# Optimization experiments

Measured on AMD Instinct MI355X. Metric: run time of the kernel, lower is better.

The kernel has to match this reference:

```python
import jax, jax.numpy as jnp
import numpy as np

N_NODES = 50000
N_EDGES = 800000
IN_FEATS = 128
OUT_FEATS = 64


def setup_inputs() -> dict:
    key = jax.random.key(0)
    k1, k2, k3, k4, k5, k6 = jax.random.split(key, 6)
    feat = jax.random.normal(k1, (N_NODES, IN_FEATS), dtype=jnp.float32)
    edge_src = jax.random.randint(k2, (N_EDGES,), 0, N_NODES, dtype=jnp.int64)
    edge_dst = jax.random.randint(k3, (N_EDGES,), 0, N_NODES, dtype=jnp.int64)
    eweight = jax.random.uniform(k4, (N_EDGES,), dtype=jnp.float32)
    W = jax.random.normal(k5, (OUT_FEATS, IN_FEATS), dtype=jnp.float32) * (1.0 / np.sqrt(IN_FEATS))
    b = jax.random.normal(k6, (OUT_FEATS,), dtype=jnp.float32) * 0.01
    return {"feat": feat, "edge_src": edge_src, "edge_dst": edge_dst,
            "eweight": eweight, "W": W, "b": b}


def reference(feat, edge_src, edge_dst, eweight, W, b):
    # Linear: [N, in] @ [in, out] + [out]
    h = jnp.einsum('ni,oi->no', feat, W) + b
    # u_mul_e: gather src features, scale by per-edge weight -> [E, out]
    m = h[edge_src] * eweight[:, None]
    # sum reduce over dst -> [N, out]
    out = jax.ops.segment_sum(m, edge_dst, num_segments=N_NODES)
    return out
```

## Files before the change

kernel.cpp:

```cpp
#include <hip/hip_runtime.h>

#define IN_FEATS 128
#define OUT_FEATS 64
#define TM 64
#define ALD 136
#define BW_LOG 6
#define BWIDTH 64
#define MAX_NB 1024
#define SE_PER_BLK 2048
#define CAP 2048
#define MAXR 4

typedef short bf16x8 __attribute__((ext_vector_type(8)));
typedef float f32x4 __attribute__((ext_vector_type(4)));

__device__ inline unsigned short f2bf(float f) {
    unsigned u = __float_as_uint(f);
    u += 0x7FFFu + ((u >> 16) & 1u);
    return (unsigned short)(u >> 16);
}
__device__ inline float bf2f_lo(unsigned v) { return __uint_as_float(v << 16); }
__device__ inline float bf2f_hi(unsigned v) { return __uint_as_float(v & 0xFFFF0000u); }
__device__ inline ushort4 cvt4(float4 t) {
    ushort4 s; s.x = f2bf(t.x); s.y = f2bf(t.y); s.z = f2bf(t.z); s.w = f2bf(t.w);
    return s;
}

__global__ __launch_bounds__(256) void stage_linear(
    const float* __restrict__ feat, const float* __restrict__ W,
    const float* __restrict__ b, unsigned short* __restrict__ h,
    const int* __restrict__ esrc, const int* __restrict__ edst,
    const float* __restrict__ ew, int* __restrict__ gcur,
    int2* __restrict__ gstage, int n_nodes, int n_edges, int nb, int nstage)
{
    __shared__ union {
        struct { unsigned short As[TM * ALD]; unsigned short Ws[OUT_FEATS * ALD]; } lin;
        struct { int cnt[MAX_NB]; int base[MAX_NB]; } st;
    } sm;
    const int tid = threadIdx.x;

    if ((int)blockIdx.x < nstage) {
        int* cnt  = sm.st.cnt;
        int* base = sm.st.base;
        for (int i = tid; i < nb; i += 256) cnt[i] = 0;
        __syncthreads();

        const int e0 = blockIdx.x * SE_PER_BLK + tid * 8;
        int dk[8]; int sk[8]; float wk[8]; int bk[8]; int rk[8];
        if (e0 + 7 < n_edges) {
            *((int4*)&dk[0]) = *((const int4*)&edst[e0]);
            *((int4*)&dk[4]) = *((const int4*)&edst[e0 + 4]);
            *((int4*)&sk[0]) = *((const int4*)&esrc[e0]);
            *((int4*)&sk[4]) = *((const int4*)&esrc[e0 + 4]);
            *((float4*)&wk[0]) = *((const float4*)&ew[e0]);
            *((float4*)&wk[4]) = *((const float4*)&ew[e0 + 4]);
#pragma unroll
            for (int i = 0; i < 8; ++i) {
                bk[i] = dk[i] >> BW_LOG;
                rk[i] = atomicAdd(&cnt[bk[i]], 1);
            }
        } else {
#pragma unroll
            for (int i = 0; i < 8; ++i) {
                int e = e0 + i;
                if (e < n_edges) {
                    dk[i] = edst[e]; sk[i] = esrc[e]; wk[i] = ew[e];
                    bk[i] = dk[i] >> BW_LOG;
                    rk[i] = atomicAdd(&cnt[bk[i]], 1);
                } else bk[i] = -1;
            }
        }
        __syncthreads();
        for (int i = tid; i < nb; i += 256) {
            int c = cnt[i];
            base[i] = c ? atomicAdd(&gcur[i], c) : 0;
        }
        __syncthreads();
#pragma unroll
        for (int i = 0; i < 8; ++i) {
            if (bk[i] >= 0) {
                int off = base[bk[i]] + rk[i];
                if (off < CAP)
                    gstage[bk[i] * CAP + off] =
                        make_int2(((dk[i] & (BWIDTH - 1)) << 16) | sk[i],
                                  __float_as_int(wk[i]));
            }
        }
    } else {
        unsigned short* As = sm.lin.As;
        unsigned short* Ws = sm.lin.Ws;
        const int row0 = ((int)blockIdx.x - nstage) * TM;

        {
            const int c  = tid & 63;
            const int kb = (tid >> 6) * 32;
            const float4* wrow = (const float4*)(W + (size_t)c * IN_FEATS + kb);
#pragma unroll
            for (int i = 0; i < 8; ++i)
                *((ushort4*)&Ws[c * ALD + kb + i * 4]) = cvt4(wrow[i]);
        }
        {
#pragma unroll
            for (int i = 0; i < 8; ++i) {
                int flat = i * 256 + tid;
                int r  = flat >> 5;
                int kc = flat & 31;
                int gr = row0 + r;
                float4 t = (gr < n_nodes)
                    ? ((const float4*)(feat + (size_t)gr * IN_FEATS))[kc]
                    : make_float4(0.f, 0.f, 0.f, 0.f);
                *((ushort4*)&As[r * ALD + kc * 4]) = cvt4(t);
            }
        }
        __syncthreads();

        const int w    = tid >> 6;
        const int lane = tid & 63;
        const int m    = lane & 15;
        const int quad = lane >> 4;
        const int koff = quad * 8;

        f32x4 acc[4];
#pragma unroll
        for (int t = 0; t < 4; ++t) acc[t] = (f32x4){0.f, 0.f, 0.f, 0.f};

#pragma unroll
        for (int chunk = 0; chunk < 4; ++chunk) {
            const int kc = chunk * 32 + koff;
            bf16x8 a = *((const bf16x8*)&As[(w * 16 + m) * ALD + kc]);
#pragma unroll
            for (int t = 0; t < 4; ++t) {
                bf16x8 bfr = *((const bf16x8*)&Ws[(t * 16 + m) * ALD + kc]);
                acc[t] = __builtin_amdgcn_mfma_f32_16x16x32_bf16(a, bfr, acc[t], 0, 0, 0);
            }
        }

#pragma unroll
        for (int t = 0; t < 4; ++t) {
            const int col = t * 16 + m;
            const float bias = b[col];
#pragma unroll
            for (int i = 0; i < 4; ++i) {
                int r = row0 + w * 16 + quad * 4 + i;
                if (r < n_nodes)
                    h[(size_t)r * OUT_FEATS + col] = f2bf(acc[t][i] + bias);
            }
        }
    }
}

__global__ __launch_bounds__(512) void sort_gather(
    const unsigned short* __restrict__ h, const int* __restrict__ gcnt,
    const int2* __restrict__ gstage, float* __restrict__ out, int n_nodes)
{
    __shared__ int2 srec[CAP];
    __shared__ int cnt[BWIDTH];
    __shared__ int cur0[BWIDTH];
    __shared__ int cur[BWIDTH];
    const int tid = threadIdx.x;
    const int b   = blockIdx.x;
    const int s0  = b * CAP;
    const int m   = min(gcnt[b], CAP);

    if (tid < BWIDTH) cnt[tid] = 0;
    __syncthreads();

    int2 rl[MAXR];
#pragma unroll
    for (int k = 0; k < MAXR; ++k) {
        int i = tid + k * 512;
        if (i < m) {
            rl[k] = gstage[s0 + i];
            atomicAdd(&cnt[(rl[k].x >> 16) & 63], 1);
        }
    }
    __syncthreads();

    if (tid < 64) {
        int v = cnt[tid];
        int inc = v;
        for (int o = 1; o < 64; o <<= 1) {
            int t = __shfl_up(inc, o, 64);
            if (tid >= o) inc += t;
        }
        int excl = inc - v;
        cur0[tid] = excl;
        cur[tid]  = excl;
    }
    __syncthreads();

#pragma unroll
    for (int k = 0; k < MAXR; ++k) {
        int i = tid + k * 512;
        if (i < m) {
            int pos = atomicAdd(&cur[(rl[k].x >> 16) & 63], 1);
            srec[pos] = rl[k];
        }
    }
    __syncthreads();

    const int lane = tid & 63;
    const int wv   = tid >> 6;
    const int g    = lane >> 4;
    const int f4   = lane & 15;
    const uint2* h64 = (const uint2*)h;

#pragma unroll
    for (int it = 0; it < 2; ++it) {
        const int nl   = wv * 8 + it * 4 + g;
        const int node = b * BWIDTH + nl;
        const int st   = cur0[nl];
        const int len  = cnt[nl];
        int omax = len;
        omax = max(omax, __shfl_xor(omax, 16, 64));
        omax = max(omax, __shfl_xor(omax, 32, 64));

        float a0 = 0.f, a1 = 0.f, a2 = 0.f, a3 = 0.f;
        for (int u = 0; u < omax; u += 8) {
            int2 r[8]; uint2 hv[8];
#pragma unroll
            for (int k = 0; k < 8; ++k) {
                int uk = u + k;
                r[k] = srec[(uk < len) ? (st + uk) : 0];
            }
#pragma unroll
            for (int k = 0; k < 8; ++k)
                hv[k] = h64[(size_t)(r[k].x & 0xFFFF) * 16 + f4];
#pragma unroll
            for (int k = 0; k < 8; ++k) {
                float w = (u + k < len) ? __int_as_float(r[k].y) : 0.f;
                a0 += w * bf2f_lo(hv[k].x);
                a1 += w * bf2f_hi(hv[k].x);
                a2 += w * bf2f_lo(hv[k].y);
                a3 += w * bf2f_hi(hv[k].y);
            }
        }
        if (node < n_nodes) {
            float4 o; o.x = a0; o.y = a1; o.z = a2; o.w = a3;
            *((float4*)&out[(size_t)node * OUT_FEATS + f4 * 4]) = o;
        }
    }
}

__global__ __launch_bounds__(256) void scatter_kernel(
    const unsigned short* __restrict__ h, const int* __restrict__ esrc,
    const int* __restrict__ edst, const float* __restrict__ ew,
    float* __restrict__ out, int n_edges)
{
    const int lane = threadIdx.x & 63;
    const int wave = threadIdx.x >> 6;
    const int stride = gridDim.x * 4;
    for (int e = blockIdx.x * 4 + wave; e < n_edges; e += stride) {
        const int s = esrc[e];
        const int d = edst[e];
        const float w = ew[e];
        atomicAdd(out + (size_t)d * OUT_FEATS + lane,
                  bf2f_lo((unsigned)h[(size_t)s * OUT_FEATS + lane]) * w);
    }
}

extern "C" void kernel_launch(void* const* d_in, const int* in_sizes, int n_in,
                              void* d_out, int out_size, void* d_ws, size_t ws_size,
                              hipStream_t stream) {
    const float* feat = (const float*)d_in[0];
    const int*   esrc = (const int*)d_in[1];
    const int*   edst = (const int*)d_in[2];
    const float* ew   = (const float*)d_in[3];
    const float* W    = (const float*)d_in[4];
    const float* b    = (const float*)d_in[5];
    float* out = (float*)d_out;

    const int n_nodes = in_sizes[0] / IN_FEATS;
    const int n_edges = in_sizes[1];
    const int nb = (n_nodes + BWIDTH - 1) >> BW_LOG;
    const int nlin = (n_nodes + TM - 1) / TM;
    const int nstage = (n_edges + SE_PER_BLK - 1) / SE_PER_BLK;

    char* wsb = (char*)d_ws;
    unsigned short* h = (unsigned short*)wsb;
    size_t off_gcur  = (((size_t)n_nodes * OUT_FEATS * sizeof(unsigned short)) + 15) & ~(size_t)15;
    size_t sz_gcur   = (((size_t)nb * sizeof(int)) + 15) & ~(size_t)15;
    size_t off_stage = off_gcur + sz_gcur;
    size_t needed    = off_stage + (size_t)nb * CAP * sizeof(int2);

    bool binnable = (nb <= MAX_NB) && (n_nodes < 65536) &&
                    ((size_t)n_edges / (size_t)nb * 3 / 2 + 300 <= CAP);

    if (ws_size >= needed && binnable) {
        int*  gcur   = (int*)(wsb + off_gcur);
        int2* gstage = (int2*)(wsb + off_stage);
        hipMemsetAsync(gcur, 0, (size_t)nb * sizeof(int), stream);
        stage_linear<<<nstage + nlin, 256, 0, stream>>>(
            feat, W, b, h, esrc, edst, ew, gcur, gstage,
            n_nodes, n_edges, nb, nstage);
        sort_gather<<<nb, 512, 0, stream>>>(h, gcur, gstage, out, n_nodes);
    } else {
        stage_linear<<<nlin, 256, 0, stream>>>(
            feat, W, b, h, esrc, edst, ew, nullptr, nullptr,
            n_nodes, n_edges, nb, 0);
        hipMemsetAsync(d_out, 0, (size_t)out_size * sizeof(float), stream);
        scatter_kernel<<<8192, 256, 0, stream>>>(h, esrc, edst, ew, out, n_edges);
    }
}
```

Before: 130.1 us.

## Split each node's edges across four lane groups and swap memset for init kernel

The gather phase used to give each 16-lane group its own node and loop to the wave-wide maximum edge count. Now all four 16-lane groups of a wave work on the same node, each taking every fourth edge two at a time, and the partial sums are combined with xor shuffles. This removes the idle lanes caused by uneven per-node degrees, at the cost of less memory-level parallelism per iteration (2 loads in flight instead of 8) and extra shuffles. The hipMemsetAsync of the cursor array is also replaced by a small one-block init kernel, which may lower launch overhead.

```diff
diff --git a/kernel.cpp b/kernel.cpp
--- a/kernel.cpp
+++ b/kernel.cpp
@@ -24,6 +24,11 @@
 __device__ inline ushort4 cvt4(float4 t) {
     ushort4 s; s.x = f2bf(t.x); s.y = f2bf(t.y); s.z = f2bf(t.z); s.w = f2bf(t.w);
     return s;
+}
+
+__global__ __launch_bounds__(256) void init_cursors(int* __restrict__ gcur, int nb)
+{
+    for (int i = threadIdx.x; i < nb; i += 256) gcur[i] = 0;
 }
 
 __global__ __launch_bounds__(256) void stage_linear(
@@ -205,37 +210,39 @@
     const int f4   = lane & 15;
     const uint2* h64 = (const uint2*)h;
 
-#pragma unroll
-    for (int it = 0; it < 2; ++it) {
-        const int nl   = wv * 8 + it * 4 + g;
+    for (int nl8 = 0; nl8 < 8; ++nl8) {
+        const int nl   = wv * 8 + nl8;
         const int node = b * BWIDTH + nl;
         const int st   = cur0[nl];
         const int len  = cnt[nl];
-        int omax = len;
-        omax = max(omax, __shfl_xor(omax, 16, 64));
-        omax = max(omax, __shfl_xor(omax, 32, 64));
 
         float a0 = 0.f, a1 = 0.f, a2 = 0.f, a3 = 0.f;
-        for (int u = 0; u < omax; u += 8) {
-            int2 r[8]; uint2 hv[8];
-#pragma unroll
-            for (int k = 0; k < 8; ++k) {
-                int uk = u + k;
-                r[k] = srec[(uk < len) ? (st + uk) : 0];
-            }
-#pragma unroll
-            for (int k = 0; k < 8; ++k)
-                hv[k] = h64[(size_t)(r[k].x & 0xFFFF) * 16 + f4];
-#pragma unroll
-            for (int k = 0; k < 8; ++k) {
-                float w = (u + k < len) ? __int_as_float(r[k].y) : 0.f;
-                a0 += w * bf2f_lo(hv[k].x);
-                a1 += w * bf2f_hi(hv[k].x);
-                a2 += w * bf2f_lo(hv[k].y);
-                a3 += w * bf2f_hi(hv[k].y);
-            }
-        }
-        if (node < n_nodes) {
+        int u = g;
+        for (; u + 4 < len; u += 8) {
+            int2 r0 = srec[st + u];
+            int2 r1 = srec[st + u + 4];
+            uint2 v0 = h64[(size_t)(r0.x & 0xFFFF) * 16 + f4];
+            uint2 v1 = h64[(size_t)(r1.x & 0xFFFF) * 16 + f4];
+            float w0 = __int_as_float(r0.y);
+            float w1 = __int_as_float(r1.y);
+            a0 += w0 * bf2f_lo(v0.x); a1 += w0 * bf2f_hi(v0.x);
+            a2 += w0 * bf2f_lo(v0.y); a3 += w0 * bf2f_hi(v0.y);
+            a0 += w1 * bf2f_lo(v1.x); a1 += w1 * bf2f_hi(v1.x);
+            a2 += w1 * bf2f_lo(v1.y); a3 += w1 * bf2f_hi(v1.y);
+        }
+        if (u < len) {
+            int2 r = srec[st + u];
+            uint2 v = h64[(size_t)(r.x & 0xFFFF) * 16 + f4];
+            float w = __int_as_float(r.y);
+            a0 += w * bf2f_lo(v.x); a1 += w * bf2f_hi(v.x);
+            a2 += w * bf2f_lo(v.y); a3 += w * bf2f_hi(v.y);
+        }
+        a0 += __shfl_xor(a0, 16, 64); a0 += __shfl_xor(a0, 32, 64);
+        a1 += __shfl_xor(a1, 16, 64); a1 += __shfl_xor(a1, 32, 64);
+        a2 += __shfl_xor(a2, 16, 64); a2 += __shfl_xor(a2, 32, 64);
+        a3 += __shfl_xor(a3, 16, 64); a3 += __shfl_xor(a3, 32, 64);
+
+        if (g == 0 && node < n_nodes) {
             float4 o; o.x = a0; o.y = a1; o.z = a2; o.w = a3;
             *((float4*)&out[(size_t)node * OUT_FEATS + f4 * 4]) = o;
         }
@@ -289,7 +296,7 @@
     if (ws_size >= needed && binnable) {
         int*  gcur   = (int*)(wsb + off_gcur);
         int2* gstage = (int2*)(wsb + off_stage);
-        hipMemsetAsync(gcur, 0, (size_t)nb * sizeof(int), stream);
+        init_cursors<<<1, 256, 0, stream>>>(gcur, nb);
         stage_linear<<<nstage + nlin, 256, 0, stream>>>(
             feat, W, b, h, esrc, edst, ew, gcur, gstage,
             n_nodes, n_edges, nb, nstage);
```

Result: faster. 126.3 us (median of 2 runs) (-2.9%).
